# Kernel tuning notes

Measured on AMD Instinct MI355X. Metric: run time of the kernel, lower is better.

## Reference

```python
import jax, jax.numpy as jnp
import numpy as np
from jax import lax

H = 2048      # hidden_size
I = 1408      # moe_inter_dim (per routed expert)
E = 16        # n_routed_experts = n_experts - n_shared
K = 4         # n_activated (top-k)
ISH = 2 * I   # shared expert intermediate = n_shared * moe_inter_dim
B, S = 4, 2048


def setup_inputs() -> dict:
    key = jax.random.key(0)
    ks = jax.random.split(key, 12)
    sc = 0.02
    return {
        "x": jax.random.normal(ks[0], (B, S, H), dtype=jnp.float32),
        # router (RouterBigger): gate/up Linear(H, E*bigger), bigger=1
        "rg_w": jax.random.normal(ks[1], (E, H), dtype=jnp.float32) * sc,
        "ru_w": jax.random.normal(ks[2], (E, H), dtype=jnp.float32) * sc,
        "extra_scale": jnp.zeros((E,), dtype=jnp.float32),  # nn.Parameter init zeros
        "extra_bias": jnp.zeros((E,), dtype=jnp.float32),   # buffer init zeros
        # stacked routed expert weights (LlamaMLP per expert)
        "Wg": jax.random.normal(ks[3], (E, I, H), dtype=jnp.float32) * sc,
        "Wu": jax.random.normal(ks[4], (E, I, H), dtype=jnp.float32) * sc,
        "Wd": jax.random.normal(ks[5], (E, H, I), dtype=jnp.float32) * sc,
        # shared expert LlamaMLP(H, n_shared*I)
        "Sg": jax.random.normal(ks[6], (ISH, H), dtype=jnp.float32) * sc,
        "Su": jax.random.normal(ks[7], (ISH, H), dtype=jnp.float32) * sc,
        "Sd": jax.random.normal(ks[8], (H, ISH), dtype=jnp.float32) * sc,
    }


def _router(xf, rg_w, ru_w, extra_scale, extra_bias):
    # scores = |up(x) * silu(gate(x))|, bigger=1 so mean over bigger axis is identity
    g = xf @ rg_w.T                              # [T, E]
    u = xf @ ru_w.T                              # [T, E]
    scores = jnp.abs(u * jax.nn.silu(g))
    probs = jax.nn.softmax(scores.astype(jnp.float32), axis=-1)  # original_scores
    biased = probs + extra_bias[None, :]
    _, idx = lax.top_k(biased, K)                # [T, K] indices
    orig = 1.0 + probs * extra_scale[None, :]
    w = jnp.take_along_axis(orig, idx, axis=1).astype(xf.dtype)  # [T, K]
    return w, idx


def reference(x, rg_w, ru_w, extra_scale, extra_bias, Wg, Wu, Wd, Sg, Su, Sd):
    shape = x.shape
    xf = x.reshape(-1, H)                        # [T, H]
    w, idx = _router(xf, rg_w, ru_w, extra_scale, extra_bias)
    # combine coefficient per (token, expert); zero if token not routed there
    coeff = jnp.einsum("tk,tke->te", w, jax.nn.one_hot(idx, E, dtype=w.dtype))  # [T, E]

    def step(y, ew):
        wg, wu, wd, c = ew                       # [I,H],[I,H],[H,I],[T]
        h = jax.nn.silu(xf @ wg.T) * (xf @ wu.T)  # [T, I]
        return y + (h @ wd.T) * c[:, None], None

    y0 = jnp.zeros_like(xf)
    y, _ = lax.scan(step, y0, (Wg, Wu, Wd, coeff.T))
    # shared experts
    z = (jax.nn.silu(xf @ Sg.T) * (xf @ Su.T)) @ Sd.T
    return (y + z).reshape(shape)
```

## Files before the change

kernel.cpp:

```cpp
#include <hip/hip_runtime.h>
#include <hip/hip_bf16.h>
#include <cmath>

#define DEVI __device__ __forceinline__

constexpr int Hn   = 2048;
constexpr int In   = 1408;
constexpr int En   = 16;
constexpr int Kn   = 4;
constexpr int ISHn = 2816;
constexpr int Tn   = 8192;
constexpr int Rn   = Tn * Kn;

typedef __attribute__((ext_vector_type(4))) float f32x4;
typedef __attribute__((ext_vector_type(8))) __bf16 bf16x8;
typedef __attribute__((ext_vector_type(8))) unsigned short u16x8;

DEVI unsigned short f2bf(float f) {
  unsigned int u = __builtin_bit_cast(unsigned int, f);
  unsigned int r = (u + 0x7fffu + ((u >> 16) & 1u)) >> 16;
  return (unsigned short)r;
}
DEVI float bf2f(unsigned short h) {
  return __builtin_bit_cast(float, (unsigned int)h << 16);
}

DEVI f32x4 mfma16(bf16x8 a, bf16x8 b, f32x4 c) {
  return __builtin_amdgcn_mfma_f32_16x16x32_bf16(a, b, c, 0, 0, 0);
}

DEVI bf16x8 lds_frag(const unsigned short* p) {
  return __builtin_bit_cast(bf16x8, *reinterpret_cast<const u16x8*>(p));
}

DEVI void gload_lds16(const void* src, void* dst) {
  __builtin_amdgcn_global_load_lds(
      (const __attribute__((address_space(1))) void*)src,
      (__attribute__((address_space(3))) void*)dst, 16, 0, 0);
}

DEVI void cvt_seg(const float* __restrict__ in, unsigned short* __restrict__ o,
                  long n8, long t0, long stride) {
  for (long v = t0; v < n8; v += stride) {
    const float4* s = reinterpret_cast<const float4*>(in + v * 8);
    float4 a = s[0], b = s[1];
    u16x8 r;
    r[0] = f2bf(a.x); r[1] = f2bf(a.y); r[2] = f2bf(a.z); r[3] = f2bf(a.w);
    r[4] = f2bf(b.x); r[5] = f2bf(b.y); r[6] = f2bf(b.z); r[7] = f2bf(b.w);
    reinterpret_cast<u16x8*>(o)[v] = r;
  }
}

__global__ __launch_bounds__(256)
void cvt_all(const float* __restrict__ x,  unsigned short* __restrict__ xb,
             const float* __restrict__ Wg, unsigned short* __restrict__ wgq,
             const float* __restrict__ Wu, unsigned short* __restrict__ wuq,
             const float* __restrict__ Wd, unsigned short* __restrict__ wdq,
             const float* __restrict__ Sg, unsigned short* __restrict__ sgq,
             const float* __restrict__ Su, unsigned short* __restrict__ suq,
             const float* __restrict__ Sd, unsigned short* __restrict__ sdq) {
  long stride = (long)gridDim.x * blockDim.x;
  long t0 = blockIdx.x * (long)blockDim.x + threadIdx.x;
  const long n8_x = (long)Tn * Hn / 8;
  const long n8_w = (long)En * In * Hn / 8;
  const long n8_s = (long)ISHn * Hn / 8;
  cvt_seg(x,  xb,  n8_x, t0, stride);
  cvt_seg(Wg, wgq, n8_w, t0, stride);
  cvt_seg(Wu, wuq, n8_w, t0, stride);
  cvt_seg(Wd, wdq, n8_w, t0, stride);
  cvt_seg(Sg, sgq, n8_s, t0, stride);
  cvt_seg(Su, suq, n8_s, t0, stride);
  cvt_seg(Sd, sdq, n8_s, t0, stride);
}

__global__ void zero_k(int* p) { p[threadIdx.x] = 0; }

__global__ __launch_bounds__(256)
void router_k(const float* __restrict__ x, const float* __restrict__ rg,
              const float* __restrict__ ru, const float* __restrict__ esc,
              const float* __restrict__ ebi, int* __restrict__ counts,
              int* __restrict__ topk, float* __restrict__ wval) {
  int w = (blockIdx.x * blockDim.x + threadIdx.x) >> 6;
  int lane = threadIdx.x & 63;
  if (w >= Tn) return;
  const float* xr = x + (size_t)w * Hn;
  float xv[Hn / 64];
#pragma unroll
  for (int j = 0; j < Hn / 64; ++j) xv[j] = xr[lane + j * 64];

  double pr[En];
  double mx = -1e300;
#pragma unroll
  for (int e = 0; e < En; ++e) {
    const float* gr = rg + (size_t)e * Hn;
    const float* ur = ru + (size_t)e * Hn;
    double pg = 0.0, pu = 0.0;
#pragma unroll
    for (int j = 0; j < Hn / 64; ++j) {
      pg += (double)xv[j] * (double)gr[lane + j * 64];
      pu += (double)xv[j] * (double)ur[lane + j * 64];
    }
#pragma unroll
    for (int s = 32; s > 0; s >>= 1) {
      pg += __shfl_xor(pg, s);
      pu += __shfl_xor(pu, s);
    }
    double sg = pg / (1.0 + exp(-pg));
    double sc = fabs(pu * sg);
    pr[e] = sc;
    mx = fmax(mx, sc);
  }
  double den = 0.0;
#pragma unroll
  for (int e = 0; e < En; ++e) { pr[e] = exp(pr[e] - mx); den += pr[e]; }

  if (lane == 0) {
    double invden = 1.0 / den;
    unsigned chosen = 0;
    for (int k = 0; k < Kn; ++k) {
      double bv = -1e300; int best = 0;
#pragma unroll
      for (int e = 0; e < En; ++e) {
        double be = pr[e] * invden + (double)ebi[e];
        if (!((chosen >> e) & 1u) && be > bv) { bv = be; best = e; }
      }
      chosen |= 1u << best;
      topk[w * Kn + k] = best;
      double pbest = bv - (double)ebi[best];
      wval[w * Kn + k] = (float)(1.0 + pbest * (double)esc[best]);
      atomicAdd(&counts[best], 1);
    }
  }
}

__global__ void prefix_k(const int* __restrict__ counts, int* __restrict__ off) {
  if (threadIdx.x == 0) {
    int a = 0;
    for (int e = 0; e < En; ++e) { off[e] = a; a += counts[e]; }
    off[En] = a;
  }
}

__global__ void build_k(const int* __restrict__ topk, const float* __restrict__ wval,
                        const int* __restrict__ off, int* __restrict__ cursor,
                        int* __restrict__ list, float* __restrict__ cw,
                        int* __restrict__ rowOf) {
  int t = blockIdx.x * blockDim.x + threadIdx.x;
  if (t >= Tn) return;
  for (int k = 0; k < Kn; ++k) {
    int e = topk[t * Kn + k];
    int pos = atomicAdd(&cursor[e], 1);
    int r = off[e] + pos;
    list[r] = t;
    cw[r] = wval[t * Kn + k];
    rowOf[t * Kn + k] = r;
  }
}


__global__ __launch_bounds__(256, 2)
void upA_k(const unsigned short* __restrict__ xb,
           const unsigned short* __restrict__ WgA, const unsigned short* __restrict__ WuA,
           const unsigned short* __restrict__ SgA, const unsigned short* __restrict__ SuA,
           const int* __restrict__ list, const int* __restrict__ off,
           const int* __restrict__ counts,
           unsigned short* __restrict__ hrt, unsigned short* __restrict__ hsh) {
  constexpr int RT = 64 * (In / 64) * En;
  int w = blockIdx.x;
  int mi, n0, Nhalf, cnt, offE;
  const unsigned short *bg, *bu;
  unsigned short* hb;
  bool gat;
  if (w < RT) {
    mi = w & 63; int rem = w >> 6;
    int ni = rem % (In / 64); int e = rem / (In / 64);
    cnt = counts[e]; offE = off[e]; Nhalf = In; n0 = ni * 64;
    size_t es = (size_t)In * Hn;
    bg = WgA + (size_t)e * es; bu = WuA + (size_t)e * es;
    hb = hrt; gat = true;
  } else {
    int w2 = w - RT;
    mi = w2 & 63; n0 = (w2 >> 6) * 64;
    cnt = Tn; offE = 0; Nhalf = ISHn;
    bg = SgA; bu = SuA; hb = hsh; gat = false;
  }
  int m0 = mi * 128;
  if (m0 >= cnt) return;

  __shared__ alignas(16) unsigned short As[128 * 64];
  __shared__ alignas(16) unsigned short Bs[128 * 64];

  int tid = threadIdx.x, lane = tid & 63, wv = tid >> 6;
  int wm = wv >> 1, wn = wv & 1;

  const unsigned short* gA[4];
  const unsigned short* gB[4];
#pragma unroll
  for (int i = 0; i < 4; ++i) {
    int idx = i * 256 + tid;
    int row = idx >> 3, ch = idx & 7;
    int sch = ch ^ (row & 7);
    int rc = m0 + row; rc = rc < cnt ? rc : cnt - 1;
    int tok = gat ? list[offE + rc] : rc;
    gA[i] = xb + (size_t)tok * Hn + sch * 8;
    const unsigned short* bb = (row < 64) ? (bg + (size_t)(n0 + row) * Hn)
                                          : (bu + (size_t)(n0 + row - 64) * Hn);
    gB[i] = bb + sch * 8;
  }

  int aOff[4], bOff[4];
#pragma unroll
  for (int m = 0; m < 4; ++m) aOff[m] = (wm * 64 + m * 16 + (lane & 15)) * 64;
#pragma unroll
  for (int n = 0; n < 4; ++n)
    bOff[n] = ((n >> 1) * 64 + wn * 32 + (n & 1) * 16 + (lane & 15)) * 64;

  f32x4 acc[4][4];
#pragma unroll
  for (int m = 0; m < 4; ++m)
#pragma unroll
    for (int n = 0; n < 4; ++n) acc[m][n] = f32x4{0.f, 0.f, 0.f, 0.f};

  for (int kb = 0; kb < Hn / 64; ++kb) {
#pragma unroll
    for (int i = 0; i < 4; ++i)
      gload_lds16(gA[i] + kb * 64, &As[i * 2048 + wv * 512]);
#pragma unroll
    for (int i = 0; i < 4; ++i)
      gload_lds16(gB[i] + kb * 64, &Bs[i * 2048 + wv * 512]);
    __syncthreads();
#pragma unroll
    for (int kk = 0; kk < 2; ++kk) {
      int soff = (((kk * 4 + (lane >> 4)) ^ (lane & 7)) << 3);
      bf16x8 a[4], b[4];
#pragma unroll
      for (int m = 0; m < 4; ++m) a[m] = lds_frag(&As[aOff[m] + soff]);
#pragma unroll
      for (int n = 0; n < 4; ++n) b[n] = lds_frag(&Bs[bOff[n] + soff]);
#pragma unroll
      for (int m = 0; m < 4; ++m)
#pragma unroll
        for (int n = 0; n < 4; ++n)
          acc[m][n] = mfma16(a[m], b[n], acc[m][n]);
    }
    __syncthreads();
  }

#pragma unroll
  for (int m = 0; m < 4; ++m) {
#pragma unroll
    for (int j = 0; j < 4; ++j) {
      int r = wm * 64 + m * 16 + (lane >> 4) * 4 + j;
      if (m0 + r < cnt) {
#pragma unroll
        for (int n = 0; n < 2; ++n) {
          int col = n0 + wn * 32 + n * 16 + (lane & 15);
          float g = acc[m][n][j], u = acc[m][n + 2][j];
          float h = (g / (1.f + __expf(-g))) * u;
          hb[(size_t)(offE + m0 + r) * Nhalf + col] = f2bf(h);
        }
      }
    }
  }
}

__global__ __launch_bounds__(256, 2)
void downA_k(const unsigned short* __restrict__ hrt, const unsigned short* __restrict__ hsh,
             const unsigned short* __restrict__ wdq, const unsigned short* __restrict__ sdq,
             const int* __restrict__ off, const int* __restrict__ counts,
             const float* __restrict__ cw,
             float* __restrict__ out, unsigned short* __restrict__ yb) {
  constexpr int NT = Hn / 128;
  constexpr int RT = 64 * NT * En;
  int w = blockIdx.x;
  int mi, n0, Kdim, cnt, offE;
  const unsigned short *bq, *hbuf;
  bool toYB;
  if (w < RT) {
    mi = w & 63; int rem = w >> 6;
    int ni = rem % NT; int e = rem / NT;
    cnt = counts[e]; offE = off[e]; Kdim = In; n0 = ni * 128;
    bq = wdq + (size_t)e * Hn * In; hbuf = hrt; toYB = true;
  } else {
    int w2 = w - RT;
    mi = w2 & 63; n0 = (w2 >> 6) * 128;
    cnt = Tn; offE = 0; Kdim = ISHn;
    bq = sdq; hbuf = hsh; toYB = false;
  }
  int m0 = mi * 128;
  if (m0 >= cnt) return;

  __shared__ alignas(16) unsigned short As[128 * 64];
  __shared__ alignas(16) unsigned short Bs[128 * 64];

  int tid = threadIdx.x, lane = tid & 63, wv = tid >> 6;
  int wm = wv >> 1, wn = wv & 1;

  const unsigned short* gA[4];
  const unsigned short* gB[4];
#pragma unroll
  for (int i = 0; i < 4; ++i) {
    int idx = i * 256 + tid;
    int row = idx >> 3, ch = idx & 7;
    int sch = ch ^ (row & 7);
    int rc = m0 + row; rc = rc < cnt ? rc : cnt - 1;
    gA[i] = hbuf + (size_t)(offE + rc) * Kdim + sch * 8;
    gB[i] = bq + (size_t)(n0 + row) * Kdim + sch * 8;
  }

  int aOff[4], bOff[4];
#pragma unroll
  for (int m = 0; m < 4; ++m) aOff[m] = (wm * 64 + m * 16 + (lane & 15)) * 64;
#pragma unroll
  for (int n = 0; n < 4; ++n) bOff[n] = (wn * 64 + n * 16 + (lane & 15)) * 64;

  f32x4 acc[4][4];
#pragma unroll
  for (int m = 0; m < 4; ++m)
#pragma unroll
    for (int n = 0; n < 4; ++n) acc[m][n] = f32x4{0.f, 0.f, 0.f, 0.f};

  int nkb = Kdim / 64;
  for (int kb = 0; kb < nkb; ++kb) {
#pragma unroll
    for (int i = 0; i < 4; ++i)
      gload_lds16(gA[i] + kb * 64, &As[i * 2048 + wv * 512]);
#pragma unroll
    for (int i = 0; i < 4; ++i)
      gload_lds16(gB[i] + kb * 64, &Bs[i * 2048 + wv * 512]);
    __syncthreads();
#pragma unroll
    for (int kk = 0; kk < 2; ++kk) {
      int soff = (((kk * 4 + (lane >> 4)) ^ (lane & 7)) << 3);
      bf16x8 a[4], b[4];
#pragma unroll
      for (int m = 0; m < 4; ++m) a[m] = lds_frag(&As[aOff[m] + soff]);
#pragma unroll
      for (int n = 0; n < 4; ++n) b[n] = lds_frag(&Bs[bOff[n] + soff]);
#pragma unroll
      for (int m = 0; m < 4; ++m)
#pragma unroll
        for (int n = 0; n < 4; ++n)
          acc[m][n] = mfma16(a[m], b[n], acc[m][n]);
    }
    __syncthreads();
  }

#pragma unroll
  for (int m = 0; m < 4; ++m) {
#pragma unroll
    for (int j = 0; j < 4; ++j) {
      int r = wm * 64 + m * 16 + (lane >> 4) * 4 + j;
      if (m0 + r < cnt) {
        float coef = 1.f;
        if (toYB) coef = cw[offE + m0 + r];
#pragma unroll
        for (int n = 0; n < 4; ++n) {
          int col = n0 + wn * 64 + n * 16 + (lane & 15);
          float v = acc[m][n][j] * coef;
          if (toYB) yb[(size_t)(offE + m0 + r) * Hn + col] = f2bf(v);
          else out[(size_t)(m0 + r) * Hn + col] = v;
        }
      }
    }
  }
}

__global__ __launch_bounds__(256)
void combine_k(const unsigned short* __restrict__ yb, const int* __restrict__ rowOf,
               float* __restrict__ out) {
  int t = blockIdx.x;
  int c = threadIdx.x * 8;
  float* op = out + (size_t)t * Hn + c;
  float4 a0 = *reinterpret_cast<float4*>(op);
  float4 a1 = *reinterpret_cast<float4*>(op + 4);
#pragma unroll
  for (int k = 0; k < Kn; ++k) {
    int r = rowOf[t * Kn + k];
    u16x8 v = *reinterpret_cast<const u16x8*>(yb + (size_t)r * Hn + c);
    a0.x += bf2f(v[0]); a0.y += bf2f(v[1]); a0.z += bf2f(v[2]); a0.w += bf2f(v[3]);
    a1.x += bf2f(v[4]); a1.y += bf2f(v[5]); a1.z += bf2f(v[6]); a1.w += bf2f(v[7]);
  }
  *reinterpret_cast<float4*>(op) = a0;
  *reinterpret_cast<float4*>(op + 4) = a1;
}

extern "C" void kernel_launch(void* const* d_in, const int* in_sizes, int n_in,
                              void* d_out, int out_size, void* d_ws, size_t ws_size,
                              hipStream_t stream) {
  const float* x   = (const float*)d_in[0];
  const float* rg  = (const float*)d_in[1];
  const float* ru  = (const float*)d_in[2];
  const float* esc = (const float*)d_in[3];
  const float* ebi = (const float*)d_in[4];
  const float* Wg  = (const float*)d_in[5];
  const float* Wu  = (const float*)d_in[6];
  const float* Wd  = (const float*)d_in[7];
  const float* Sg  = (const float*)d_in[8];
  const float* Su  = (const float*)d_in[9];
  const float* Sd  = (const float*)d_in[10];
  float* out = (float*)d_out;

  char* ws = (char*)d_ws;

  const size_t sz_xb  = (size_t)Tn * Hn * 2;
  const size_t sz_wgu = (size_t)En * In * Hn * 2;
  const size_t sz_sgu = (size_t)ISHn * Hn * 2;
  const size_t sz_hrt = (size_t)Rn * In * 2;
  const size_t sz_hsh = (size_t)Tn * ISHn * 2;
  const size_t sz_misc = 1 << 20;

  size_t o = 0;
  auto take = [&](size_t b) { size_t r = o; o += (b + 255) & ~(size_t)255; return r; };
  size_t o_xb  = take(sz_xb);
  size_t o_wg  = take(sz_wgu);
  size_t o_wu  = take(sz_wgu);
  size_t o_wd  = take(sz_wgu);
  size_t o_sg  = take(sz_sgu);
  size_t o_su  = take(sz_sgu);
  size_t o_sd  = take(sz_sgu);
  size_t o_hrt = take(sz_hrt);
  size_t o_hsh = take(sz_hsh);
  size_t o_mi  = take(sz_misc);

  unsigned short* xb  = (unsigned short*)(ws + o_xb);
  unsigned short* wgq = (unsigned short*)(ws + o_wg);
  unsigned short* wuq = (unsigned short*)(ws + o_wu);
  unsigned short* wdq = (unsigned short*)(ws + o_wd);
  unsigned short* sgq = (unsigned short*)(ws + o_sg);
  unsigned short* suq = (unsigned short*)(ws + o_su);
  unsigned short* sdq = (unsigned short*)(ws + o_sd);
  unsigned short* hrt = (unsigned short*)(ws + o_hrt);
  unsigned short* hsh = (unsigned short*)(ws + o_hsh);
  char* misc = ws + o_mi;
  int*   counts = (int*)(misc);
  int*   cursor = (int*)(misc + 64);
  int*   off    = (int*)(misc + 128);
  int*   topk   = (int*)(misc + 256);
  float* wval   = (float*)(misc + 256 + 131072);
  int*   list   = (int*)(misc + 256 + 2 * 131072);
  float* cw     = (float*)(misc + 256 + 3 * 131072);
  int*   rowOf  = (int*)(misc + 256 + 4 * 131072);
  unsigned short* yb = wgq;

  zero_k<<<1, 32, 0, stream>>>(counts);
  router_k<<<2048, 256, 0, stream>>>(x, rg, ru, esc, ebi, counts, topk, wval);
  cvt_all<<<2048, 256, 0, stream>>>(x, xb, Wg, wgq, Wu, wuq, Wd, wdq,
                                    Sg, sgq, Su, suq, Sd, sdq);
  prefix_k<<<1, 64, 0, stream>>>(counts, off);
  build_k<<<Tn / 256, 256, 0, stream>>>(topk, wval, off, cursor, list, cw, rowOf);

  upA_k<<<64 * (In / 64) * En + 64 * (ISHn / 64), 256, 0, stream>>>(
      xb, wgq, wuq, sgq, suq, list, off, counts, hrt, hsh);
  downA_k<<<64 * (Hn / 128) * En + 64 * (Hn / 128), 256, 0, stream>>>(
      hrt, hsh, wdq, sdq, off, counts, cw, out, yb);
  combine_k<<<Tn, 256, 0, stream>>>(yb, rowOf, out);
}
```

Before: 1.894 ms.

## Fuse x bf16 cast into router and group GEMM block order for L2 reuse

The router kernel, which already loads each token row of x, now writes the bf16 copy of x as well, so the conversion kernel no longer reads x a second time. The block-index decoding in the up and down GEMM kernels is changed from M-fastest ordering to groups of 8 M-tiles swept across N tiles. Blocks running at the same time then share A and B tiles in L2, cutting repeated global reads. The router's writes are strided per lane, which may coalesce less well than the vectorized conversion path.

```diff
diff --git a/kernel.cpp b/kernel.cpp
--- a/kernel.cpp
+++ b/kernel.cpp
@@ -52,8 +52,7 @@
 }
 
 __global__ __launch_bounds__(256)
-void cvt_all(const float* __restrict__ x,  unsigned short* __restrict__ xb,
-             const float* __restrict__ Wg, unsigned short* __restrict__ wgq,
+void cvt_all(const float* __restrict__ Wg, unsigned short* __restrict__ wgq,
              const float* __restrict__ Wu, unsigned short* __restrict__ wuq,
              const float* __restrict__ Wd, unsigned short* __restrict__ wdq,
              const float* __restrict__ Sg, unsigned short* __restrict__ sgq,
@@ -61,10 +60,8 @@
              const float* __restrict__ Sd, unsigned short* __restrict__ sdq) {
   long stride = (long)gridDim.x * blockDim.x;
   long t0 = blockIdx.x * (long)blockDim.x + threadIdx.x;
-  const long n8_x = (long)Tn * Hn / 8;
   const long n8_w = (long)En * In * Hn / 8;
   const long n8_s = (long)ISHn * Hn / 8;
-  cvt_seg(x,  xb,  n8_x, t0, stride);
   cvt_seg(Wg, wgq, n8_w, t0, stride);
   cvt_seg(Wu, wuq, n8_w, t0, stride);
   cvt_seg(Wd, wdq, n8_w, t0, stride);
@@ -79,7 +76,8 @@
 void router_k(const float* __restrict__ x, const float* __restrict__ rg,
               const float* __restrict__ ru, const float* __restrict__ esc,
               const float* __restrict__ ebi, int* __restrict__ counts,
-              int* __restrict__ topk, float* __restrict__ wval) {
+              int* __restrict__ topk, float* __restrict__ wval,
+              unsigned short* __restrict__ xb) {
   int w = (blockIdx.x * blockDim.x + threadIdx.x) >> 6;
   int lane = threadIdx.x & 63;
   if (w >= Tn) return;
@@ -87,6 +85,10 @@
   float xv[Hn / 64];
 #pragma unroll
   for (int j = 0; j < Hn / 64; ++j) xv[j] = xr[lane + j * 64];
+
+  unsigned short* xbr = xb + (size_t)w * Hn;
+#pragma unroll
+  for (int j = 0; j < Hn / 64; ++j) xbr[lane + j * 64] = f2bf(xv[j]);
 
   double pr[En];
   double mx = -1e300;
@@ -165,23 +167,31 @@
            const int* __restrict__ list, const int* __restrict__ off,
            const int* __restrict__ counts,
            unsigned short* __restrict__ hrt, unsigned short* __restrict__ hsh) {
-  constexpr int RT = 64 * (In / 64) * En;
+  constexpr int NTr = In / 64;
+  constexpr int RT  = En * NTr * 64;
   int w = blockIdx.x;
   int mi, n0, Nhalf, cnt, offE;
   const unsigned short *bg, *bu;
   unsigned short* hb;
   bool gat;
   if (w < RT) {
-    mi = w & 63; int rem = w >> 6;
-    int ni = rem % (In / 64); int e = rem / (In / 64);
+    int e  = w / (NTr * 64);
+    int r  = w - e * (NTr * 64);
+    int mg = r / (NTr * 8);
+    int r2 = r - mg * (NTr * 8);
+    int ni = r2 >> 3, m8 = r2 & 7;
+    mi = (mg << 3) | m8;
     cnt = counts[e]; offE = off[e]; Nhalf = In; n0 = ni * 64;
     size_t es = (size_t)In * Hn;
     bg = WgA + (size_t)e * es; bu = WuA + (size_t)e * es;
     hb = hrt; gat = true;
   } else {
     int w2 = w - RT;
-    mi = w2 & 63; n0 = (w2 >> 6) * 64;
-    cnt = Tn; offE = 0; Nhalf = ISHn;
+    int mg = w2 / (44 * 8);
+    int r2 = w2 - mg * (44 * 8);
+    int ni = r2 >> 3, m8 = r2 & 7;
+    mi = (mg << 3) | m8;
+    cnt = Tn; offE = 0; Nhalf = ISHn; n0 = ni * 64;
     bg = SgA; bu = SuA; hb = hsh; gat = false;
   }
   int m0 = mi * 128;
@@ -271,20 +281,27 @@
              const float* __restrict__ cw,
              float* __restrict__ out, unsigned short* __restrict__ yb) {
   constexpr int NT = Hn / 128;
-  constexpr int RT = 64 * NT * En;
+  constexpr int RT = En * NT * 64;
   int w = blockIdx.x;
   int mi, n0, Kdim, cnt, offE;
   const unsigned short *bq, *hbuf;
   bool toYB;
   if (w < RT) {
-    mi = w & 63; int rem = w >> 6;
-    int ni = rem % NT; int e = rem / NT;
+    int e  = w >> 10;
+    int r  = w & 1023;
+    int mg = r >> 7;
+    int r2 = r & 127;
+    int ni = r2 >> 3, m8 = r2 & 7;
+    mi = (mg << 3) | m8;
     cnt = counts[e]; offE = off[e]; Kdim = In; n0 = ni * 128;
     bq = wdq + (size_t)e * Hn * In; hbuf = hrt; toYB = true;
   } else {
     int w2 = w - RT;
-    mi = w2 & 63; n0 = (w2 >> 6) * 128;
-    cnt = Tn; offE = 0; Kdim = ISHn;
+    int mg = w2 >> 7;
+    int r2 = w2 & 127;
+    int ni = r2 >> 3, m8 = r2 & 7;
+    mi = (mg << 3) | m8;
+    cnt = Tn; offE = 0; Kdim = ISHn; n0 = ni * 128;
     bq = sdq; hbuf = hsh; toYB = false;
   }
   int m0 = mi * 128;
@@ -444,15 +461,15 @@
   unsigned short* yb = wgq;
 
   zero_k<<<1, 32, 0, stream>>>(counts);
-  router_k<<<2048, 256, 0, stream>>>(x, rg, ru, esc, ebi, counts, topk, wval);
-  cvt_all<<<2048, 256, 0, stream>>>(x, xb, Wg, wgq, Wu, wuq, Wd, wdq,
+  router_k<<<2048, 256, 0, stream>>>(x, rg, ru, esc, ebi, counts, topk, wval, xb);
+  cvt_all<<<2048, 256, 0, stream>>>(Wg, wgq, Wu, wuq, Wd, wdq,
                                     Sg, sgq, Su, suq, Sd, sdq);
   prefix_k<<<1, 64, 0, stream>>>(counts, off);
   build_k<<<Tn / 256, 256, 0, stream>>>(topk, wval, off, cursor, list, cw, rowOf);
 
-  upA_k<<<64 * (In / 64) * En + 64 * (ISHn / 64), 256, 0, stream>>>(
+  upA_k<<<En * (In / 64) * 64 + 64 * (ISHn / 64), 256, 0, stream>>>(
       xb, wgq, wuq, sgq, suq, list, off, counts, hrt, hsh);
-  downA_k<<<64 * (Hn / 128) * En + 64 * (Hn / 128), 256, 0, stream>>>(
+  downA_k<<<En * (Hn / 128) * 64 + 64 * (Hn / 128), 256, 0, stream>>>(
       hrt, hsh, wdq, sdq, off, counts, cw, out, yb);
   combine_k<<<Tn, 256, 0, stream>>>(yb, rowOf, out);
 }
```

New measurement: 1.706 ms, median of 2. 1.11x faster.
